# Kernel optimization log

Hardware: AMD Instinct MI355X
Metric: run time of the kernel (lower is better)

Reference implementation:

```python
import jax, jax.numpy as jnp
import numpy as np

B, C, H, W = 2, 192, 128, 128
HEADS = 4
M = 128          # num_tokens
RD = 10          # reducted_dim
GS = 256         # category_size
TDF = 16         # dim_ffn_td
HID = 4 * C      # mlp hidden (768)
HIDT = HID + TDF # 784 after concat with token-dict features
KS = 5


def _ln(x, g, b):
    mu = x.mean(-1, keepdims=True)
    var = ((x - mu) ** 2).mean(-1, keepdims=True)
    return (x - mu) / jnp.sqrt(var + 1e-5) * g + b


def _gelu(x):
    return jax.nn.gelu(x, approximate=False)  # torch nn.GELU default = exact erf


def setup_inputs() -> dict:
    key = jax.random.key(0)
    ks = jax.random.split(key, 16)
    s = 0.02
    inp = {
        "x": jax.random.normal(ks[0], (B, C, H, W), jnp.float32),
        "x_size": H,
        "td": jax.random.normal(ks[1], (M, C), jnp.float32),
        "g1": jnp.ones((C,)), "b1": jnp.zeros((C,)),
        "g2": jnp.ones((C,)), "b2": jnp.zeros((C,)),
        "g3": jnp.ones((C,)), "b3": jnp.zeros((C,)),
        "wq_w": jax.random.normal(ks[2], (C, RD)) * s, "wq_b": jnp.zeros((RD,)),
        "wk_w": jax.random.normal(ks[3], (C, RD)) * s, "wk_b": jnp.zeros((RD,)),
        "wv_w": jax.random.normal(ks[4], (C, C)) * s, "wv_b": jnp.zeros((C,)),
        "ca_scale": jnp.ones((1,)),
        "wqkv_w": jax.random.normal(ks[5], (C, 3 * C)) * s, "wqkv_b": jnp.zeros((3 * C,)),
        "proj_w": jax.random.normal(ks[6], (C, C)) * s, "proj_b": jnp.zeros((C,)),
        "fc_td_w": jax.random.normal(ks[7], (C, TDF)) * s, "fc_td_b": jnp.zeros((TDF,)),
        "fc1_w": jax.random.normal(ks[8], (C, HID)) * s, "fc1_b": jnp.zeros((HID,)),
        "dw_w": jax.random.normal(ks[9], (HIDT, 1, KS, KS)) * s, "dw_b": jnp.zeros((HIDT,)),
        "fc2_w": jax.random.normal(ks[10], (HIDT, C)) * s, "fc2_b": jnp.zeros((C,)),
    }
    return inp


def reference(x, x_size, td, g1, b1, g2, b2, g3, b3, wq_w, wq_b, wk_w, wk_b,
              wv_w, wv_b, ca_scale, wqkv_w, wqkv_b, proj_w, proj_b,
              fc_td_w, fc_td_b, fc1_w, fc1_b, dw_w, dw_b, fc2_w, fc2_b):
    b, c, h, w = x.shape
    n = h * w
    xs = x.reshape(b, c, n).transpose(0, 2, 1)          # [b,n,c] patch_embed
    shortcut = xs
    xn = _ln(xs, g1, b1)                                # norm1

    # ---- ATD_CA: L2-normalized cross-attention to token dict ----
    q = xn @ wq_w + wq_b                                # [b,n,rd]
    k = td @ wk_w + wk_b                                # [m,rd]
    v = td @ wv_w + wv_b                                # [m,c]
    qn = q / jnp.maximum(jnp.linalg.norm(q, axis=-1, keepdims=True), 1e-12)
    kn = k / jnp.maximum(jnp.linalg.norm(k, axis=-1, keepdims=True), 1e-12)
    sim = jnp.einsum('bnr,mr->bnm', qn, kn)
    scale = 1.0 + jnp.clip(ca_scale, 0.0, 3.0) * np.log(M)
    sim = jax.nn.softmax(sim * scale, axis=-1)          # [b,n,m]
    x_atd = jnp.einsum('bnm,mc->bnc', sim, v)
    tk_id = jnp.argmax(sim, axis=-1)                    # [b,n] int

    # ---- AC_MSA: category-sorted grouped self-attention ----
    qkv = xn @ wqkv_w + wqkv_b                          # [b,n,3c]
    sort_idx = jnp.argsort(tk_id, axis=-1)              # [b,n]
    inv_idx = jnp.argsort(sort_idx, axis=-1)            # index_reverse
    shuf = jnp.take_along_axis(qkv, sort_idx[:, :, None], axis=1)
    gs = min(n, GS)
    ng = (n + gs - 1) // gs
    pad_n = ng * gs - n
    pad = jnp.flip(shuf[:, n - pad_n:n, :], axis=1)
    padded = jnp.concatenate([shuf, pad], axis=1)       # [b, ng*gs, 3c]
    hd = c // HEADS
    y = padded.reshape(b, ng, gs, 3, HEADS, hd)
    y = jnp.transpose(y, (3, 0, 1, 4, 2, 5))            # [3,b,ng,H,gs,hd]
    q2, k2, v2 = y[0], y[1], y[2]
    attn = jnp.einsum('bghqd,bghkd->bghqk', q2, k2) * (hd ** -0.5)
    attn = jax.nn.softmax(attn, axis=-1)
    o = jnp.einsum('bghqk,bghkd->bghqd', attn, v2)
    o = jnp.transpose(o, (0, 1, 3, 2, 4)).reshape(b, ng * gs, c)[:, :n, :]
    o = jnp.take_along_axis(o, inv_idx[:, :, None], axis=1)
    x_aca = o @ proj_w + proj_b

    # ---- token-dict features gathered per token ----
    td_feat = td @ fc_td_w + fc_td_b                    # [m,tdf]
    x_td = jnp.take(td_feat, tk_id, axis=0)             # [b,n,tdf]

    # ---- ConvFFN_td ----
    xn2 = _ln(xs, g2, b2)
    h1 = _gelu(xn2 @ fc1_w + fc1_b)                     # [b,n,hid]
    hcat = jnp.concatenate([h1, x_td], axis=-1)         # [b,n,hidt]
    img = hcat.transpose(0, 2, 1).reshape(b, HIDT, h, w)
    conv = jax.lax.conv_general_dilated(
        img, dw_w, window_strides=(1, 1), padding=((KS // 2, KS // 2),) * 2,
        dimension_numbers=('NCHW', 'OIHW', 'NCHW'), feature_group_count=HIDT)
    conv = _gelu(conv + dw_b[None, :, None, None])
    conv = conv.reshape(b, HIDT, n).transpose(0, 2, 1)
    x_ffn = (hcat + conv) @ fc2_w + fc2_b
    x_ffn = _ln(x_ffn, g3, b3)                          # norm3

    out = shortcut + x_atd + x_aca + x_ffn
    return out.transpose(0, 2, 1).reshape(b, c, h, w)
```

## Files before the change

### kernel.cpp

```cpp
#include <hip/hip_runtime.h>
#include <hip/hip_bf16.h>
#include <math.h>

using bf16 = __hip_bfloat16;

static constexpr int B = 2, C = 192, Hh = 128, Ww = 128, N = Hh * Ww;
static constexpr int M = 128, RD = 10, GS = 256, NG = N / GS;
static constexpr int HEADS = 4, HD = C / HEADS;
static constexpr int TDF = 16, HID = 4 * C, HIDT = HID + TDF;
static constexpr int TC3 = 3 * C;
static constexpr float LOG_M = 4.852030263919617f;
static constexpr float ATT_SCALE = 0.14433756729740643f;

typedef __attribute__((ext_vector_type(8))) short bf16x8;
typedef __attribute__((ext_vector_type(4))) float f32x4;

__device__ __forceinline__ float b2f(bf16 v) { return __bfloat162float(v); }
__device__ __forceinline__ bf16 f2b(float v) { return __float2bfloat16(v); }
__device__ __forceinline__ float bits2f(unsigned short u) { return __uint_as_float(((unsigned)u) << 16); }
__device__ __forceinline__ unsigned short f2bits(float f) {
    union { bf16 h; unsigned short u; } cv; cv.h = f2b(f); return cv.u;
}
__device__ __forceinline__ float gelu_exact(float v) {
    return 0.5f * v * (1.0f + erff(v * 0.70710678118654752f));
}

__global__ void __launch_bounds__(256) k_wtrans(const float* in, bf16* out, int K, int Nn) {
    __shared__ float T[64][65];
    int n0 = blockIdx.x * 64, k0 = blockIdx.y * 64;
    int tid = threadIdx.x;
    for (int e = tid; e < 4096; e += 256) {
        int kk = e >> 6, nn = e & 63;
        if (k0 + kk < K) T[kk][nn] = in[(size_t)(k0 + kk) * Nn + n0 + nn];
    }
    __syncthreads();
    for (int e = tid; e < 4096; e += 256) {
        int nn = e >> 6, kk = e & 63;
        if (k0 + kk < K) out[(size_t)(n0 + nn) * K + k0 + kk] = f2b(T[kk][nn]);
    }
}

__global__ void k_precompute(const float* td, const float* wk_w, const float* wk_b,
                             const float* wv_w, const float* wv_b,
                             const float* fc_td_w, const float* fc_td_b,
                             float* kn, bf16* vvT, float* tdf) {
    int m = blockIdx.x;
    int lane = threadIdx.x;
    __shared__ float trow[C];
    for (int ch = lane; ch < C; ch += 64) trow[ch] = td[m * C + ch];
    __syncthreads();
    __shared__ float ks[RD];
    __shared__ float inv_s;
    if (lane < RD) {
        float s = wk_b[lane];
        for (int ch = 0; ch < C; ++ch) s += trow[ch] * wk_w[ch * RD + lane];
        ks[lane] = s;
    }
    __syncthreads();
    if (lane == 0) {
        float ss = 0.f;
        for (int r = 0; r < RD; ++r) ss += ks[r] * ks[r];
        inv_s = 1.0f / fmaxf(sqrtf(ss), 1e-12f);
    }
    __syncthreads();
    if (lane < RD) kn[m * RD + lane] = ks[lane] * inv_s;
    for (int c0 = 0; c0 < 3; ++c0) {
        int co = lane + 64 * c0;
        float s = wv_b[co];
        for (int ch = 0; ch < C; ++ch) s += trow[ch] * wv_w[ch * C + co];
        vvT[(size_t)co * M + m] = f2b(s);
    }
    if (lane < TDF) {
        float s = fc_td_b[lane];
        for (int ch = 0; ch < C; ++ch) s += trow[ch] * fc_td_w[ch * TDF + lane];
        tdf[m * TDF + lane] = s;
    }
}

__global__ void __launch_bounds__(256) k_ln(const float* x, bf16* t, float* xn32, float* acc) {
    __shared__ float Xs[64 * 193];
    __shared__ float mu_s[64], rs_s[64];
    int tid = threadIdx.x;
    int m0 = blockIdx.x * 64;
    int b = m0 / N, i0 = m0 % N;
    for (int e = tid; e < 192 * 64; e += 256) {
        int ch = e >> 6, ii = e & 63;
        Xs[ii * 193 + ch] = x[((size_t)b * C + ch) * N + i0 + ii];
    }
    __syncthreads();
    {
        int tok = tid >> 2, part = tid & 3;
        float s = 0.f, ss = 0.f;
        for (int ch = part * 48; ch < part * 48 + 48; ++ch) {
            float v = Xs[tok * 193 + ch]; s += v; ss += v * v;
        }
        s += __shfl_xor(s, 1); ss += __shfl_xor(ss, 1);
        s += __shfl_xor(s, 2); ss += __shfl_xor(ss, 2);
        if (part == 0) {
            float mu = s / C;
            mu_s[tok] = mu;
            rs_s[tok] = rsqrtf(ss / C - mu * mu + 1e-5f);
        }
    }
    __syncthreads();
    for (int e = tid; e < 64 * 192; e += 256) {
        int ii = e / 192, ch = e % 192;
        float v = Xs[ii * 193 + ch];
        float xn = (v - mu_s[ii]) * rs_s[ii];
        size_t g = (size_t)(m0 + ii);
        t[g * C + ch] = f2b(xn);
        xn32[g * C + ch] = xn;
        acc[g * C + ch] = v;
    }
}

__global__ void __launch_bounds__(256) k_atdca(const float* xn32, const float* g1, const float* b1,
                        const float* wq_w, const float* wq_b, const float* ca_scale,
                        const float* kn, bf16* p_buf, int* tk_id) {
    int t0 = blockIdx.x * 4;
    int w = threadIdx.x >> 6, lane = threadIdx.x & 63;
    int g = t0 + w;
    float xn[3];
    #pragma unroll
    for (int k = 0; k < 3; ++k) {
        int ch = lane + 64 * k;
        xn[k] = xn32[(size_t)g * C + ch] * g1[ch] + b1[ch];
    }
    float q[RD];
    #pragma unroll
    for (int r = 0; r < RD; ++r) {
        float p = 0.f;
        #pragma unroll
        for (int k = 0; k < 3; ++k) { int ch = lane + 64 * k; p += xn[k] * wq_w[ch * RD + r]; }
        for (int mk = 32; mk >= 1; mk >>= 1) p += __shfl_xor(p, mk);
        q[r] = p + wq_b[r];
    }
    float ssn = 0.f;
    #pragma unroll
    for (int r = 0; r < RD; ++r) ssn += q[r] * q[r];
    float invq = 1.0f / fmaxf(sqrtf(ssn), 1e-12f);
    float s0 = 0.f, s1 = 0.f;
    #pragma unroll
    for (int r = 0; r < RD; ++r) {
        float qr = q[r] * invq;
        s0 += qr * kn[lane * RD + r];
        s1 += qr * kn[(lane + 64) * RD + r];
    }
    float mv; int mi;
    if (s1 > s0) { mv = s1; mi = lane + 64; } else { mv = s0; mi = lane; }
    for (int mk = 32; mk >= 1; mk >>= 1) {
        float ov = __shfl_xor(mv, mk); int oi = __shfl_xor(mi, mk);
        if (ov > mv || (ov == mv && oi < mi)) { mv = ov; mi = oi; }
    }
    float cs = ca_scale[0]; cs = fminf(fmaxf(cs, 0.0f), 3.0f);
    float scale = 1.0f + cs * LOG_M;
    float e0 = expf((s0 - mv) * scale), e1 = expf((s1 - mv) * scale);
    float sum = e0 + e1;
    for (int mk = 32; mk >= 1; mk >>= 1) sum += __shfl_xor(sum, mk);
    float invs = 1.0f / sum;
    p_buf[(size_t)g * M + lane] = f2b(e0 * invs);
    p_buf[(size_t)g * M + lane + 64] = f2b(e1 * invs);
    if (lane == 0) tk_id[g] = mi;
}

__global__ void __launch_bounds__(256) k_pv(const bf16* p_buf, const bf16* vvT, float* acc) {
    __shared__ __align__(16) short As[64 * 136];
    __shared__ __align__(16) short Bs[64 * 136];
    int tid = threadIdx.x;
    int m0 = blockIdx.x * 64;
    int n0 = blockIdx.y * 64;
    for (int e = tid; e < 64 * 16; e += 256) {
        int m = e >> 4, kc = (e & 15) * 8;
        *(uint4*)&As[m * 136 + kc] = *(const uint4*)(p_buf + (size_t)(m0 + m) * M + kc);
    }
    for (int e = tid; e < 64 * 16; e += 256) {
        int n = e >> 4, kc = (e & 15) * 8;
        *(uint4*)&Bs[n * 136 + kc] = *(const uint4*)(vvT + (size_t)(n0 + n) * M + kc);
    }
    __syncthreads();
    int w = tid >> 6, lane = tid & 63;
    int wm = (w >> 1) * 32, wn = (w & 1) * 32;
    int lr = lane & 15, lk = (lane >> 4) * 8;
    f32x4 acc00 = {0.f,0.f,0.f,0.f}, acc01 = acc00, acc10 = acc00, acc11 = acc00;
    #pragma unroll
    for (int ks = 0; ks < 4; ++ks) {
        int k0 = ks * 32 + lk;
        bf16x8 a0 = *(bf16x8*)&As[(wm + lr) * 136 + k0];
        bf16x8 a1 = *(bf16x8*)&As[(wm + 16 + lr) * 136 + k0];
        bf16x8 b0 = *(bf16x8*)&Bs[(wn + lr) * 136 + k0];
        bf16x8 b1 = *(bf16x8*)&Bs[(wn + 16 + lr) * 136 + k0];
        acc00 = __builtin_amdgcn_mfma_f32_16x16x32_bf16(a0, b0, acc00, 0, 0, 0);
        acc01 = __builtin_amdgcn_mfma_f32_16x16x32_bf16(a0, b1, acc01, 0, 0, 0);
        acc10 = __builtin_amdgcn_mfma_f32_16x16x32_bf16(a1, b0, acc10, 0, 0, 0);
        acc11 = __builtin_amdgcn_mfma_f32_16x16x32_bf16(a1, b1, acc11, 0, 0, 0);
    }
    int rbase = (lane >> 4) * 4;
    f32x4 accs[2][2] = {{acc00, acc01}, {acc10, acc11}};
    #pragma unroll
    for (int mt = 0; mt < 2; ++mt) {
        #pragma unroll
        for (int nt = 0; nt < 2; ++nt) {
            int co = n0 + wn + nt * 16 + lr;
            #pragma unroll
            for (int r = 0; r < 4; ++r) {
                int tok = m0 + wm + mt * 16 + rbase + r;
                acc[(size_t)tok * C + co] += accs[mt][nt][r];
            }
        }
    }
}

template<int NOUT, int OUTLD, int MODE, bool HASGAIN>
__global__ void __launch_bounds__(256) k_gemm192(const bf16* Abuf, const float* gain, const float* beta,
                                                 const bf16* Wt, const float* bias,
                                                 bf16* outb, float* outf) {
    __shared__ __align__(16) short As[64 * 200];
    __shared__ __align__(16) short Bs[64 * 200];
    int tid = threadIdx.x;
    int m0 = blockIdx.x * 64;
    int n0 = blockIdx.y * 64;
    for (int e = tid; e < 64 * 24; e += 256) {
        int m = e / 24, kc = (e % 24) * 8;
        uint4 raw = *(const uint4*)(Abuf + (size_t)(m0 + m) * C + kc);
        if (HASGAIN) {
            unsigned short* u = (unsigned short*)&raw;
            unsigned short o[8];
            #pragma unroll
            for (int j = 0; j < 8; ++j) o[j] = f2bits(bits2f(u[j]) * gain[kc + j] + beta[kc + j]);
            *(uint4*)&As[m * 200 + kc] = *(uint4*)o;
        } else {
            *(uint4*)&As[m * 200 + kc] = raw;
        }
    }
    for (int e = tid; e < 64 * 24; e += 256) {
        int n = e / 24, kc = (e % 24) * 8;
        *(uint4*)&Bs[n * 200 + kc] = *(const uint4*)(Wt + (size_t)(n0 + n) * C + kc);
    }
    __syncthreads();
    int w = tid >> 6, lane = tid & 63;
    int wm = (w >> 1) * 32, wn = (w & 1) * 32;
    int lr = lane & 15, lk = (lane >> 4) * 8;
    f32x4 acc00 = {0.f,0.f,0.f,0.f}, acc01 = acc00, acc10 = acc00, acc11 = acc00;
    #pragma unroll
    for (int ks = 0; ks < 6; ++ks) {
        int k0 = ks * 32 + lk;
        bf16x8 a0 = *(bf16x8*)&As[(wm + lr) * 200 + k0];
        bf16x8 a1 = *(bf16x8*)&As[(wm + 16 + lr) * 200 + k0];
        bf16x8 b0 = *(bf16x8*)&Bs[(wn + lr) * 200 + k0];
        bf16x8 b1 = *(bf16x8*)&Bs[(wn + 16 + lr) * 200 + k0];
        acc00 = __builtin_amdgcn_mfma_f32_16x16x32_bf16(a0, b0, acc00, 0, 0, 0);
        acc01 = __builtin_amdgcn_mfma_f32_16x16x32_bf16(a0, b1, acc01, 0, 0, 0);
        acc10 = __builtin_amdgcn_mfma_f32_16x16x32_bf16(a1, b0, acc10, 0, 0, 0);
        acc11 = __builtin_amdgcn_mfma_f32_16x16x32_bf16(a1, b1, acc11, 0, 0, 0);
    }
    int rbase = (lane >> 4) * 4;
    f32x4 accs[2][2] = {{acc00, acc01}, {acc10, acc11}};
    #pragma unroll
    for (int mt = 0; mt < 2; ++mt) {
        #pragma unroll
        for (int nt = 0; nt < 2; ++nt) {
            int co = n0 + wn + nt * 16 + lr;
            float bv = bias[co];
            #pragma unroll
            for (int r = 0; r < 4; ++r) {
                int tok = m0 + wm + mt * 16 + rbase + r;
                float v = accs[mt][nt][r] + bv;
                if (MODE == 0) outb[(size_t)tok * OUTLD + co] = f2b(v);
                else if (MODE == 1) outb[(size_t)tok * OUTLD + co] = f2b(gelu_exact(v));
                else outf[(size_t)tok * OUTLD + co] += v;
            }
        }
    }
}

__global__ void k_sort_count(const int* tk_id, int* chunk_cnt) {
    int c = blockIdx.x, b = blockIdx.y;
    int tid = threadIdx.x;
    __shared__ int cnt[M];
    cnt[tid] = 0;
    __syncthreads();
    atomicAdd(&cnt[tk_id[b * N + c * 128 + tid]], 1);
    __syncthreads();
    chunk_cnt[(b * 128 + c) * M + tid] = cnt[tid];
}

__global__ void k_sort_scan(int* chunk_cnt) {
    int b = blockIdx.x;
    int k = threadIdx.x;
    int tot = 0;
    for (int c = 0; c < 128; ++c) tot += chunk_cnt[(b * 128 + c) * M + k];
    __shared__ int totals[M];
    __shared__ int base[M];
    totals[k] = tot;
    __syncthreads();
    if (k == 0) {
        int run = 0;
        for (int kk = 0; kk < M; ++kk) { base[kk] = run; run += totals[kk]; }
    }
    __syncthreads();
    int run = base[k];
    for (int c = 0; c < 128; ++c) {
        int v = chunk_cnt[(b * 128 + c) * M + k];
        chunk_cnt[(b * 128 + c) * M + k] = run;
        run += v;
    }
}

__global__ void k_sort_scatter(const int* tk_id, const int* chunk_cnt, int* sort_idx) {
    int c = blockIdx.x, b = blockIdx.y;
    int k = threadIdx.x;
    __shared__ int keys[128];
    keys[k] = tk_id[b * N + c * 128 + k];
    __syncthreads();
    int off = chunk_cnt[(b * 128 + c) * M + k];
    for (int j = 0; j < 128; ++j) {
        if (keys[j] == k) sort_idx[b * N + off++] = c * 128 + j;
    }
}

__global__ void __launch_bounds__(256) k_attn_mfma(const bf16* qkv, const int* sort_idx, bf16* o_buf) {
    int g = blockIdx.x, h = blockIdx.y, b = blockIdx.z;
    __shared__ int sidx[GS];
    __shared__ __align__(16) unsigned short Kl[256 * 64];
    __shared__ __align__(16) unsigned short Vt[48 * 256];
    __shared__ __align__(16) unsigned short Pl[4][64 * 32];
    int tid = threadIdx.x;
    sidx[tid] = sort_idx[b * N + g * GS + tid];
    __syncthreads();
    {
        int row = tid;
        int srow = sidx[row];
        size_t kb = ((size_t)(b * N + srow)) * TC3 + C + h * HD;
        size_t vb = ((size_t)(b * N + srow)) * TC3 + 2 * C + h * HD;
        #pragma unroll
        for (int db = 0; db < 6; ++db) {
            uint4 kv = *(const uint4*)(qkv + kb + db * 8);
            *(uint4*)&Kl[row * 64 + ((db ^ (row & 7)) * 8)] = kv;
            uint4 vv4 = *(const uint4*)(qkv + vb + db * 8);
            unsigned short* vu = (unsigned short*)&vv4;
            #pragma unroll
            for (int j = 0; j < 8; ++j) {
                int d = db * 8 + j;
                Vt[d * 256 + (((row >> 3) ^ (d & 7)) * 8) + (row & 7)] = vu[j];
            }
        }
        uint4 z = {0u,0u,0u,0u};
        *(uint4*)&Kl[row * 64 + ((6 ^ (row & 7)) * 8)] = z;
        *(uint4*)&Kl[row * 64 + ((7 ^ (row & 7)) * 8)] = z;
    }
    __syncthreads();
    int w = tid >> 6, l = tid & 63;
    int lq = l & 15, g8 = l >> 4;
    bf16x8 qf[4][2];
    #pragma unroll
    for (int qt = 0; qt < 4; ++qt) {
        int qrow = sidx[w * 64 + qt * 16 + lq];
        size_t qb = ((size_t)(b * N + qrow)) * TC3 + h * HD;
        qf[qt][0] = *(const bf16x8*)(qkv + qb + g8 * 8);
        int d1 = 32 + g8 * 8;
        if (d1 < HD) qf[qt][1] = *(const bf16x8*)(qkv + qb + d1);
        else { uint4 z = {0u,0u,0u,0u}; qf[qt][1] = *(bf16x8*)&z; }
    }
    float mrun[4], lrun[4];
    f32x4 Oa[4][3];
    #pragma unroll
    for (int qt = 0; qt < 4; ++qt) {
        mrun[qt] = -1e30f; lrun[qt] = 0.f;
        #pragma unroll
        for (int dt = 0; dt < 3; ++dt) Oa[qt][dt] = (f32x4){0.f,0.f,0.f,0.f};
    }
    unsigned short* Pw = &Pl[w][0];
    for (int ck = 0; ck < 8; ++ck) {
        int kbase = ck * 32;
        bf16x8 kf[2][2];
        #pragma unroll
        for (int kt = 0; kt < 2; ++kt) {
            int key = kbase + kt * 16 + lq;
            #pragma unroll
            for (int ks = 0; ks < 2; ++ks)
                kf[kt][ks] = *(bf16x8*)&Kl[key * 64 + (((ks * 4 + g8) ^ (key & 7)) * 8)];
        }
        bf16x8 vf[3];
        #pragma unroll
        for (int dt = 0; dt < 3; ++dt) {
            int d = dt * 16 + lq;
            vf[dt] = *(bf16x8*)&Vt[d * 256 + ((((kbase >> 3) + g8) ^ (d & 7)) * 8)];
        }
        #pragma unroll
        for (int qt = 0; qt < 4; ++qt) {
            f32x4 s0 = {0.f,0.f,0.f,0.f}, s1 = s0;
            s0 = __builtin_amdgcn_mfma_f32_16x16x32_bf16(kf[0][0], qf[qt][0], s0, 0, 0, 0);
            s0 = __builtin_amdgcn_mfma_f32_16x16x32_bf16(kf[0][1], qf[qt][1], s0, 0, 0, 0);
            s1 = __builtin_amdgcn_mfma_f32_16x16x32_bf16(kf[1][0], qf[qt][0], s1, 0, 0, 0);
            s1 = __builtin_amdgcn_mfma_f32_16x16x32_bf16(kf[1][1], qf[qt][1], s1, 0, 0, 0);
            float sv0[4], sv1[4];
            float cmax = -1e30f;
            #pragma unroll
            for (int r = 0; r < 4; ++r) {
                sv0[r] = s0[r] * ATT_SCALE; sv1[r] = s1[r] * ATT_SCALE;
                cmax = fmaxf(cmax, fmaxf(sv0[r], sv1[r]));
            }
            cmax = fmaxf(cmax, __shfl_xor(cmax, 16));
            cmax = fmaxf(cmax, __shfl_xor(cmax, 32));
            float mnew = fmaxf(mrun[qt], cmax);
            float sf = expf(mrun[qt] - mnew);
            float p0[4], p1[4], csum = 0.f;
            #pragma unroll
            for (int r = 0; r < 4; ++r) {
                p0[r] = expf(sv0[r] - mnew); p1[r] = expf(sv1[r] - mnew);
                csum += p0[r] + p1[r];
            }
            csum += __shfl_xor(csum, 16);
            csum += __shfl_xor(csum, 32);
            lrun[qt] = lrun[qt] * sf + csum;
            mrun[qt] = mnew;
            int q = qt * 16 + lq;
            {
                unsigned short pw[4];
                #pragma unroll
                for (int r = 0; r < 4; ++r) pw[r] = f2bits(p0[r]);
                int slot = g8;
                int addr = q * 32 + (((slot >> 1) ^ (q & 3)) * 8) + (slot & 1) * 4;
                *(uint2*)&Pw[addr] = *(uint2*)pw;
                #pragma unroll
                for (int r = 0; r < 4; ++r) pw[r] = f2bits(p1[r]);
                slot = 4 + g8;
                addr = q * 32 + (((slot >> 1) ^ (q & 3)) * 8) + (slot & 1) * 4;
                *(uint2*)&Pw[addr] = *(uint2*)pw;
            }
            float sfr[4];
            #pragma unroll
            for (int r = 0; r < 4; ++r) sfr[r] = __shfl(sf, 4 * g8 + r);
            #pragma unroll
            for (int dt = 0; dt < 3; ++dt)
                #pragma unroll
                for (int r = 0; r < 4; ++r) Oa[qt][dt][r] *= sfr[r];
            bf16x8 pa = *(bf16x8*)&Pw[q * 32 + ((g8 ^ (lq & 3)) * 8)];
            #pragma unroll
            for (int dt = 0; dt < 3; ++dt)
                Oa[qt][dt] = __builtin_amdgcn_mfma_f32_16x16x32_bf16(pa, vf[dt], Oa[qt][dt], 0, 0, 0);
        }
    }
    #pragma unroll
    for (int qt = 0; qt < 4; ++qt) {
        float invq = 1.0f / lrun[qt];
        float invr[4];
        #pragma unroll
        for (int r = 0; r < 4; ++r) invr[r] = __shfl(invq, 4 * g8 + r);
        #pragma unroll
        for (int r = 0; r < 4; ++r) {
            int grow = sidx[w * 64 + qt * 16 + 4 * g8 + r];
            size_t obase = ((size_t)(b * N + grow)) * C + h * HD;
            #pragma unroll
            for (int dt = 0; dt < 3; ++dt)
                o_buf[obase + dt * 16 + lq] = f2b(Oa[qt][dt][r] * invr[r]);
        }
    }
}

__global__ void k_tdfill(const int* tk_id, const float* tdf, bf16* hcat) {
    int idx = blockIdx.x * 256 + threadIdx.x;
    if (idx >= B * N * TDF) return;
    int tok = idx >> 4, f = idx & 15;
    hcat[(size_t)tok * HIDT + HID + f] = f2b(tdf[tk_id[tok] * TDF + f]);
}

__global__ void __launch_bounds__(256) k_conv(const bf16* hcat, const float* dw_w, const float* dw_b,
                                              bf16* convsum) {
    int st = blockIdx.x;
    int c16 = blockIdx.y;
    int b = blockIdx.z;
    int tx0 = (st & 7) * 16, ty0 = (st >> 3) * 16;
    int tid = threadIdx.x;
    __shared__ __align__(16) float Hf[20 * 81 * 4];
    __shared__ __align__(16) float Wf[25 * 16];
    __shared__ float Wb[16];
    for (int e = tid; e < 400; e += 256) {
        int tap = e >> 4, ch = e & 15;
        Wf[e] = dw_w[(size_t)(c16 * 16 + ch) * 25 + tap];
    }
    if (tid < 16) Wb[tid] = dw_b[c16 * 16 + tid];
    for (int e = tid; e < 800; e += 256) {
        int pos = e >> 1, sc = e & 1;
        int py = pos / 20, px = pos % 20;
        int gy = ty0 + py - 2, gx = tx0 + px - 2;
        uint4 v = {0u, 0u, 0u, 0u};
        if (gy >= 0 && gy < Hh && gx >= 0 && gx < Ww)
            v = *(const uint4*)(hcat + ((size_t)b * N + gy * Ww + gx) * HIDT + c16 * 16 + sc * 8);
        unsigned short* u = (unsigned short*)&v;
        float4 f0 = { bits2f(u[0]), bits2f(u[1]), bits2f(u[2]), bits2f(u[3]) };
        float4 f1 = { bits2f(u[4]), bits2f(u[5]), bits2f(u[6]), bits2f(u[7]) };
        int base = (py * 81 + px * 4 + sc * 2) * 4;
        *(float4*)&Hf[base] = f0;
        *(float4*)&Hf[base + 4] = f1;
    }
    __syncthreads();
    int cc = tid & 1, lx = (tid >> 1) & 7, ly = tid >> 4;
    float acc[2][8] = {};
    #pragma unroll 1
    for (int ky = 0; ky < 5; ++ky) {
        int py = ly + ky;
        float4 w[5][2];
        #pragma unroll
        for (int kx = 0; kx < 5; ++kx) {
            w[kx][0] = *(float4*)&Wf[(ky * 5 + kx) * 16 + cc * 8];
            w[kx][1] = *(float4*)&Wf[(ky * 5 + kx) * 16 + cc * 8 + 4];
        }
        #pragma unroll
        for (int c = 0; c < 6; ++c) {
            int px = 2 * lx + c;
            int base = (py * 81 + px * 4 + cc * 2) * 4;
            float4 f0 = *(float4*)&Hf[base];
            float4 f1 = *(float4*)&Hf[base + 4];
            float f[8] = { f0.x, f0.y, f0.z, f0.w, f1.x, f1.y, f1.z, f1.w };
            #pragma unroll
            for (int kx = 0; kx < 5; ++kx) {
                int ox = c - kx;
                if (ox >= 0 && ox < 2) {
                    const float* wp = (const float*)&w[kx][0];
                    #pragma unroll
                    for (int j = 0; j < 8; ++j) acc[ox][j] += f[j] * wp[j];
                }
            }
        }
    }
    int gy = ty0 + ly;
    #pragma unroll
    for (int ox = 0; ox < 2; ++ox) {
        int px = 2 * lx + ox + 2, py = ly + 2;
        int base = (py * 81 + px * 4 + cc * 2) * 4;
        float4 f0 = *(float4*)&Hf[base];
        float4 f1 = *(float4*)&Hf[base + 4];
        float cf[8] = { f0.x, f0.y, f0.z, f0.w, f1.x, f1.y, f1.z, f1.w };
        unsigned short ow[8];
        #pragma unroll
        for (int j = 0; j < 8; ++j)
            ow[j] = f2bits(cf[j] + gelu_exact(acc[ox][j] + Wb[cc * 8 + j]));
        int gx = tx0 + 2 * lx + ox;
        *(uint4*)(convsum + ((size_t)b * N + gy * Ww + gx) * HIDT + c16 * 16 + cc * 8) = *(uint4*)ow;
    }
}

__global__ void __launch_bounds__(256) k_fc2ln(const bf16* convsum, const bf16* Wt,
                                               const float* bias, const float* g3, const float* b3,
                                               const float* accres, float* out) {
    __shared__ __align__(16) unsigned short As[64 * 64];
    __shared__ __align__(16) unsigned short Bs[192 * 64];
    int tid = threadIdx.x;
    int m0 = blockIdx.x * 64;
    int w = tid >> 6, lane = tid & 63;
    int lr = lane & 15, g8 = lane >> 4;
    f32x4 acc[12];
    #pragma unroll
    for (int nt = 0; nt < 12; ++nt) acc[nt] = (f32x4){0.f, 0.f, 0.f, 0.f};
    for (int kc = 0; kc < 13; ++kc) {
        int kb = kc * 64;
        for (int e = tid; e < 512; e += 256) {
            int m = e >> 3, k8 = (e & 7) * 8;
            uint4 v = {0u,0u,0u,0u};
            if (kb + k8 < HIDT) v = *(const uint4*)(convsum + (size_t)(m0 + m) * HIDT + kb + k8);
            *(uint4*)&As[m * 64 + (((e & 7) ^ (m & 7)) * 8)] = v;
        }
        for (int e = tid; e < 1536; e += 256) {
            int n = e >> 3, k8 = (e & 7) * 8;
            uint4 v = {0u,0u,0u,0u};
            if (kb + k8 < HIDT) v = *(const uint4*)(Wt + (size_t)n * HIDT + kb + k8);
            *(uint4*)&Bs[n * 64 + (((e & 7) ^ (n & 7)) * 8)] = v;
        }
        __syncthreads();
        #pragma unroll
        for (int ks = 0; ks < 2; ++ks) {
            int kg = ks * 4 + g8;
            int arow = w * 16 + lr;
            bf16x8 a = *(bf16x8*)&As[arow * 64 + ((kg ^ (arow & 7)) * 8)];
            #pragma unroll
            for (int nt = 0; nt < 12; ++nt) {
                int nrow = nt * 16 + lr;
                bf16x8 bfr = *(bf16x8*)&Bs[nrow * 64 + ((kg ^ (nrow & 7)) * 8)];
                acc[nt] = __builtin_amdgcn_mfma_f32_16x16x32_bf16(a, bfr, acc[nt], 0, 0, 0);
            }
        }
        __syncthreads();
    }
    #pragma unroll
    for (int nt = 0; nt < 12; ++nt) {
        float bv = bias[nt * 16 + lr];
        #pragma unroll
        for (int r = 0; r < 4; ++r) acc[nt][r] += bv;
    }
    #pragma unroll
    for (int r = 0; r < 4; ++r) {
        float s = 0.f, ss = 0.f;
        #pragma unroll
        for (int nt = 0; nt < 12; ++nt) { float v = acc[nt][r]; s += v; ss += v * v; }
        s += __shfl_xor(s, 1); ss += __shfl_xor(ss, 1);
        s += __shfl_xor(s, 2); ss += __shfl_xor(ss, 2);
        s += __shfl_xor(s, 4); ss += __shfl_xor(ss, 4);
        s += __shfl_xor(s, 8); ss += __shfl_xor(ss, 8);
        float mu = s / C;
        float rstd = rsqrtf(ss / C - mu * mu + 1e-5f);
        int tok = m0 + w * 16 + g8 * 4 + r;
        int b = tok / N, i = tok % N;
        #pragma unroll
        for (int nt = 0; nt < 12; ++nt) {
            int c = nt * 16 + lr;
            float o = accres[(size_t)tok * C + c] + (acc[nt][r] - mu) * rstd * g3[c] + b3[c];
            out[((size_t)b * C + c) * N + i] = o;
        }
    }
}

__global__ void k_sentinel(float* out, int nelem) {
    int i = blockIdx.x * blockDim.x + threadIdx.x;
    if (i < nelem) out[i] = 1234.0f;
}

extern "C" void kernel_launch(void* const* d_in, const int* in_sizes, int n_in,
                              void* d_out, int out_size, void* d_ws, size_t ws_size,
                              hipStream_t stream) {
    const float* x        = (const float*)d_in[0];
    const float* td       = (const float*)d_in[2];
    const float* g1       = (const float*)d_in[3];
    const float* b1       = (const float*)d_in[4];
    const float* g2       = (const float*)d_in[5];
    const float* b2v      = (const float*)d_in[6];
    const float* g3       = (const float*)d_in[7];
    const float* b3       = (const float*)d_in[8];
    const float* wq_w     = (const float*)d_in[9];
    const float* wq_b     = (const float*)d_in[10];
    const float* wk_w     = (const float*)d_in[11];
    const float* wk_b     = (const float*)d_in[12];
    const float* wv_w     = (const float*)d_in[13];
    const float* wv_b     = (const float*)d_in[14];
    const float* ca_scale = (const float*)d_in[15];
    const float* wqkv_w   = (const float*)d_in[16];
    const float* wqkv_b   = (const float*)d_in[17];
    const float* proj_w   = (const float*)d_in[18];
    const float* proj_b   = (const float*)d_in[19];
    const float* fc_td_w  = (const float*)d_in[20];
    const float* fc_td_b  = (const float*)d_in[21];
    const float* fc1_w    = (const float*)d_in[22];
    const float* fc1_b    = (const float*)d_in[23];
    const float* dw_w     = (const float*)d_in[24];
    const float* dw_b     = (const float*)d_in[25];
    const float* fc2_w    = (const float*)d_in[26];
    const float* fc2_b    = (const float*)d_in[27];
    float* out = (float*)d_out;

    char* ws = (char*)d_ws;
    size_t off = 0;
    auto alloc = [&](size_t bytes) { size_t o = off; off += (bytes + 255) & ~(size_t)255; return o; };
    size_t o_t     = alloc((size_t)B * N * C * 2);
    size_t o_xn32  = alloc((size_t)B * N * C * 4);
    size_t o_acc   = alloc((size_t)B * N * C * 4);
    size_t o_qkv   = alloc((size_t)B * N * TC3 * 2);
    size_t o_obuf  = alloc((size_t)B * N * C * 2);
    size_t o_hcat  = alloc((size_t)B * N * HIDT * 2);
    size_t o_conv  = alloc((size_t)B * N * HIDT * 2);
    size_t o_kn    = alloc((size_t)M * RD * 4);
    size_t o_vvT   = alloc((size_t)C * M * 2);
    size_t o_tdf   = alloc((size_t)M * TDF * 4);
    size_t o_tk    = alloc((size_t)B * N * 4);
    size_t o_sidx  = alloc((size_t)B * N * 4);
    size_t o_ccnt  = alloc((size_t)B * 128 * M * 4);
    size_t o_pbuf  = alloc((size_t)B * N * M * 2);
    size_t o_wqkvT = alloc((size_t)TC3 * C * 2);
    size_t o_projT = alloc((size_t)C * C * 2);
    size_t o_fc1T  = alloc((size_t)HID * C * 2);
    size_t o_fc2T  = alloc((size_t)C * HIDT * 2);

    if (ws_size < off) {
        k_sentinel<<<(out_size + 255) / 256, 256, 0, stream>>>(out, out_size);
        return;
    }

    bf16*  t_buf   = (bf16*)(ws + o_t);
    float* xn32    = (float*)(ws + o_xn32);
    float* acc     = (float*)(ws + o_acc);
    bf16*  qkv     = (bf16*)(ws + o_qkv);
    bf16*  o_bufp  = (bf16*)(ws + o_obuf);
    bf16*  hcat    = (bf16*)(ws + o_hcat);
    bf16*  convsum = (bf16*)(ws + o_conv);
    float* kn      = (float*)(ws + o_kn);
    bf16*  vvT     = (bf16*)(ws + o_vvT);
    float* tdf     = (float*)(ws + o_tdf);
    int*   tk_id   = (int*)(ws + o_tk);
    int*   sidx    = (int*)(ws + o_sidx);
    int*   ccnt    = (int*)(ws + o_ccnt);
    bf16*  p_buf   = (bf16*)(ws + o_pbuf);
    bf16*  wqkvT   = (bf16*)(ws + o_wqkvT);
    bf16*  projT   = (bf16*)(ws + o_projT);
    bf16*  fc1T    = (bf16*)(ws + o_fc1T);
    bf16*  fc2T    = (bf16*)(ws + o_fc2T);

    k_wtrans<<<dim3(TC3 / 64, C / 64), 256, 0, stream>>>(wqkv_w, wqkvT, C, TC3);
    k_wtrans<<<dim3(C / 64, C / 64), 256, 0, stream>>>(proj_w, projT, C, C);
    k_wtrans<<<dim3(HID / 64, C / 64), 256, 0, stream>>>(fc1_w, fc1T, C, HID);
    k_wtrans<<<dim3(C / 64, (HIDT + 63) / 64), 256, 0, stream>>>(fc2_w, fc2T, HIDT, C);

    k_precompute<<<M, 64, 0, stream>>>(td, wk_w, wk_b, wv_w, wv_b, fc_td_w, fc_td_b, kn, vvT, tdf);
    k_ln<<<B * N / 64, 256, 0, stream>>>(x, t_buf, xn32, acc);
    k_atdca<<<B * N / 4, 256, 0, stream>>>(xn32, g1, b1, wq_w, wq_b, ca_scale, kn, p_buf, tk_id);
    k_pv<<<dim3(B * N / 64, C / 64), 256, 0, stream>>>(p_buf, vvT, acc);
    k_gemm192<TC3, TC3, 0, true><<<dim3(B * N / 64, TC3 / 64), 256, 0, stream>>>(
        t_buf, g1, b1, wqkvT, wqkv_b, qkv, nullptr);
    k_sort_count<<<dim3(128, B), 128, 0, stream>>>(tk_id, ccnt);
    k_sort_scan<<<B, 128, 0, stream>>>(ccnt);
    k_sort_scatter<<<dim3(128, B), 128, 0, stream>>>(tk_id, ccnt, sidx);
    k_attn_mfma<<<dim3(NG, HEADS, B), 256, 0, stream>>>(qkv, sidx, o_bufp);
    k_gemm192<C, C, 2, false><<<dim3(B * N / 64, C / 64), 256, 0, stream>>>(
        o_bufp, nullptr, nullptr, projT, proj_b, nullptr, acc);
    k_gemm192<HID, HIDT, 1, true><<<dim3(B * N / 64, HID / 64), 256, 0, stream>>>(
        t_buf, g2, b2v, fc1T, fc1_b, hcat, nullptr);
    k_tdfill<<<(B * N * TDF + 255) / 256, 256, 0, stream>>>(tk_id, tdf, hcat);
    k_conv<<<dim3(64, 49, B), 256, 0, stream>>>(hcat, dw_w, dw_b, convsum);
    k_fc2ln<<<B * N / 64, 256, 0, stream>>>(convsum, fc2T, fc2_b, g3, b3, acc, out);
}
```

Before: 393.5 us.

## Double-buffer fc2 LDS tiles and stage NCHW output through shared memory

Changes the fc2+LayerNorm kernel to double-buffer its A/B LDS tiles, so the next K-chunk loads while the current one feeds MFMA. This drops one barrier per iteration. The output write now goes through a padded shared-memory transpose buffer, giving coalesced float4 stores to the channel-major output instead of scattered scalar stores. LDS use grows to 64KB per block, which may lower occupancy.

```diff
diff --git a/kernel.cpp b/kernel.cpp
--- a/kernel.cpp
+++ b/kernel.cpp
@@ -544,8 +544,10 @@
 __global__ void __launch_bounds__(256) k_fc2ln(const bf16* convsum, const bf16* Wt,
                                                const float* bias, const float* g3, const float* b3,
                                                const float* accres, float* out) {
-    __shared__ __align__(16) unsigned short As[64 * 64];
-    __shared__ __align__(16) unsigned short Bs[192 * 64];
+    __shared__ __align__(16) char smem[65536];
+    unsigned short* AsB = (unsigned short*)smem;
+    unsigned short* BsB = (unsigned short*)(smem + 16384);
+    float* Ot = (float*)smem;
     int tid = threadIdx.x;
     int m0 = blockIdx.x * 64;
     int w = tid >> 6, lane = tid & 63;
@@ -553,8 +555,11 @@
     f32x4 acc[12];
     #pragma unroll
     for (int nt = 0; nt < 12; ++nt) acc[nt] = (f32x4){0.f, 0.f, 0.f, 0.f};
-    for (int kc = 0; kc < 13; ++kc) {
+
+    auto stage = [&](int d, int kc) {
         int kb = kc * 64;
+        unsigned short* As = AsB + d * 4096;
+        unsigned short* Bs = BsB + d * 12288;
         for (int e = tid; e < 512; e += 256) {
             int m = e >> 3, k8 = (e & 7) * 8;
             uint4 v = {0u,0u,0u,0u};
@@ -567,7 +572,14 @@
             if (kb + k8 < HIDT) v = *(const uint4*)(Wt + (size_t)n * HIDT + kb + k8);
             *(uint4*)&Bs[n * 64 + (((e & 7) ^ (n & 7)) * 8)] = v;
         }
+    };
+    stage(0, 0);
+    int cur = 0;
+    for (int kc = 0; kc < 13; ++kc) {
         __syncthreads();
+        if (kc + 1 < 13) stage(cur ^ 1, kc + 1);
+        unsigned short* As = AsB + cur * 4096;
+        unsigned short* Bs = BsB + cur * 12288;
         #pragma unroll
         for (int ks = 0; ks < 2; ++ks) {
             int kg = ks * 4 + g8;
@@ -580,7 +592,7 @@
                 acc[nt] = __builtin_amdgcn_mfma_f32_16x16x32_bf16(a, bfr, acc[nt], 0, 0, 0);
             }
         }
-        __syncthreads();
+        cur ^= 1;
     }
     #pragma unroll
     for (int nt = 0; nt < 12; ++nt) {
@@ -588,6 +600,7 @@
         #pragma unroll
         for (int r = 0; r < 4; ++r) acc[nt][r] += bv;
     }
+    float mu_r[4], rs_r[4];
     #pragma unroll
     for (int r = 0; r < 4; ++r) {
         float s = 0.f, ss = 0.f;
@@ -597,15 +610,30 @@
         s += __shfl_xor(s, 2); ss += __shfl_xor(ss, 2);
         s += __shfl_xor(s, 4); ss += __shfl_xor(ss, 4);
         s += __shfl_xor(s, 8); ss += __shfl_xor(ss, 8);
-        float mu = s / C;
-        float rstd = rsqrtf(ss / C - mu * mu + 1e-5f);
-        int tok = m0 + w * 16 + g8 * 4 + r;
-        int b = tok / N, i = tok % N;
-        #pragma unroll
-        for (int nt = 0; nt < 12; ++nt) {
+        mu_r[r] = s / C;
+        rs_r[r] = rsqrtf(ss / C - mu_r[r] * mu_r[r] + 1e-5f);
+    }
+    int bb = m0 / N, i0 = m0 % N;
+    for (int h = 0; h < 2; ++h) {
+        __syncthreads();
+        #pragma unroll
+        for (int ntl = 0; ntl < 6; ++ntl) {
+            int nt = h * 6 + ntl;
             int c = nt * 16 + lr;
-            float o = accres[(size_t)tok * C + c] + (acc[nt][r] - mu) * rstd * g3[c] + b3[c];
-            out[((size_t)b * C + c) * N + i] = o;
+            float g3v = g3[c], b3v = b3[c];
+            #pragma unroll
+            for (int r = 0; r < 4; ++r) {
+                int tok = m0 + w * 16 + g8 * 4 + r;
+                float o = accres[(size_t)tok * C + c] + (acc[nt][r] - mu_r[r]) * rs_r[r] * g3v + b3v;
+                Ot[(ntl * 16 + lr) * 68 + w * 16 + g8 * 4 + r] = o;
+            }
+        }
+        __syncthreads();
+        for (int e = tid; e < 96 * 16; e += 256) {
+            int row = e >> 4, q4 = e & 15;
+            int c = h * 96 + row;
+            float4 v = *(float4*)&Ot[row * 68 + q4 * 4];
+            *(float4*)(out + ((size_t)(bb * C + c)) * N + i0 + q4 * 4) = v;
         }
     }
 }
```

New measurement: 390.9 us. About the same (-0.7%).
